# Performance work log

Hardware: AMD Instinct MI355X
Metric: run time of the kernel (lower is better)

Reference implementation:

```python
import jax, jax.numpy as jnp
import numpy as np

E = 8        # n_routed_experts
K = 2        # n_experts_per_token
H = 1024     # d_hidden
D = 512      # d_expert
NSH = 2      # n_shared_experts -> shared expert width = D*NSH


def setup_inputs() -> dict:
    key = jax.random.key(0)
    ks = jax.random.split(key, 8)
    s = 0.02
    x = jax.random.normal(ks[0], (4, 2048, H), jnp.float32)
    W_router = (jax.random.normal(ks[1], (H, E), jnp.float32) * s)
    Wg = (jax.random.normal(ks[2], (E, H, D), jnp.float32) * s)   # per-expert gate proj
    Wu = (jax.random.normal(ks[3], (E, H, D), jnp.float32) * s)   # per-expert up proj
    Wd = (jax.random.normal(ks[4], (E, D, H), jnp.float32) * s)   # per-expert down proj
    Ds = D * NSH
    Wsg = (jax.random.normal(ks[5], (H, Ds), jnp.float32) * s)
    Wsu = (jax.random.normal(ks[6], (H, Ds), jnp.float32) * s)
    Wsd = (jax.random.normal(ks[7], (Ds, H), jnp.float32) * s)
    return {"x": x, "W_router": W_router, "Wg": Wg, "Wu": Wu, "Wd": Wd,
            "Wsg": Wsg, "Wsu": Wsu, "Wsd": Wsd}


def reference(x, W_router, Wg, Wu, Wd, Wsg, Wsu, Wsd):
    B, S, Hd = x.shape
    T = B * S
    xf = x.reshape(T, Hd)

    # shared expert (SwiGLU)
    shared = (jax.nn.silu(xf @ Wsg) * (xf @ Wsu)) @ Wsd          # [T, H]

    # gating: softmax -> top-k -> renormalize
    logits = xf @ W_router                                        # [T, E]
    probs = jax.nn.softmax(logits, axis=-1)
    topk_scores, topk_idx = jax.lax.top_k(probs, K)               # [T, K]
    topk_scores = topk_scores / jnp.sum(topk_scores, axis=-1, keepdims=True)

    # combine weights: zero for unselected experts (topk indices are distinct,
    # so the original's first-match score selection equals a simple scatter)
    combine = jnp.zeros((T, E), x.dtype).at[jnp.arange(T)[:, None], topk_idx].set(topk_scores)

    # per-expert SwiGLU, computed densely and combined with sparse weights
    gate = jax.nn.silu(jnp.einsum('th,ehd->etd', xf, Wg))         # [E, T, D]
    up = jnp.einsum('th,ehd->etd', xf, Wu)                        # [E, T, D]
    expert_out = jnp.einsum('etd,edh->eth', gate * up, Wd)        # [E, T, H]
    routed = jnp.einsum('eth,te->th', expert_out, combine)        # [T, H]

    out = (routed + shared).reshape(B, S, Hd)

    # load-balancing aux loss: E * sum(mean_probs^2)
    probs_mean = jnp.mean(probs.reshape(B, S, E), axis=(0, 1))
    aux_loss = E * jnp.sum(probs_mean * probs_mean)
    return out, aux_loss
```

## Files before the change

kernel.cpp:

```cpp
#include <hip/hip_runtime.h>


typedef unsigned short u16;
typedef unsigned int   u32;
typedef short short8 __attribute__((ext_vector_type(8)));
typedef float f32x4  __attribute__((ext_vector_type(4)));

#define AS1 __attribute__((address_space(1)))
#define AS3 __attribute__((address_space(3)))

constexpr int T  = 8192;
constexpr int H  = 1024;
constexpr int E  = 8;
constexpr int D  = 512;
constexpr int DS = 1024;
constexpr int PAIR_CAP  = 17408;
constexpr int MT_ROUTED = 136;
constexpr int RB = 256;

__device__ __forceinline__ u16 f2bf(float f){
  u32 u = __builtin_bit_cast(u32, f);
  u += 0x7fffu + ((u >> 16) & 1u);
  return (u16)(u >> 16);
}
__device__ __forceinline__ float bf2f(u16 h){
  u32 u = ((u32)h) << 16;
  return __builtin_bit_cast(float, u);
}

__device__ __forceinline__ void gl_lds16(const u16* g, u16* l){
  __builtin_amdgcn_global_load_lds((const AS1 void*)g, (AS3 void*)l, 16, 0, 0);
}

template<int ROWS>
__device__ __forceinline__ void stage_tile(const u16* __restrict__ gbase, int ld, int k0,
                                           int rowbase, const int* __restrict__ gather,
                                           u16* lds, int wave, int lane){
  constexpr int ISS = ROWS / 32;
  int lr = lane >> 3, ch = lane & 7;
  int chs = (ch ^ lr) * 8;
#pragma unroll
  for (int j = 0; j < ISS; ++j){
    int idx = wave * ISS + j;
    int row = idx * 8 + lr;
    int grow = gather ? gather[rowbase + row] : (rowbase + row);
    const u16* g = gbase + (long)grow * ld + k0 + chs;
    gl_lds16(g, lds + idx * 512);
  }
}

__device__ __forceinline__ int swz_off(int c, int lane){
  return ((c ^ (lane & 7)) * 8);
}

__global__ void __launch_bounds__(256) router_kernel(
    const float* __restrict__ x, const float* __restrict__ Wr,
    u16* __restrict__ xb,
    int* __restrict__ topk_idx, float* __restrict__ topk_w,
    int* __restrict__ partial_hist, float* __restrict__ partial_probs)
{
  __shared__ int   hist_s[4][8];
  __shared__ float ps_s[4][8];
  int tid = threadIdx.x, lane = tid & 63, wv = tid >> 6;
  int   histl[8] = {0,0,0,0,0,0,0,0};
  float psl[8]   = {0.f,0.f,0.f,0.f,0.f,0.f,0.f,0.f};

  for (int it = 0; it < 8; ++it){
    int t = blockIdx.x * 32 + wv * 8 + it;
    const float4* xr = (const float4*)(x + (long)t * H);
    uint2* xbr = (uint2*)(xb + (long)t * H);
    float acc[8];
#pragma unroll
    for (int e = 0; e < 8; ++e) acc[e] = 0.f;
#pragma unroll
    for (int i = 0; i < 4; ++i){
      float4 xv = xr[i * 64 + lane];
      u32 lo = (u32)f2bf(xv.x) | ((u32)f2bf(xv.y) << 16);
      u32 hi = (u32)f2bf(xv.z) | ((u32)f2bf(xv.w) << 16);
      xbr[i * 64 + lane] = make_uint2(lo, hi);
      int h0 = i * 256 + lane * 4;
#pragma unroll
      for (int j = 0; j < 4; ++j){
        float xs = (j == 0) ? xv.x : (j == 1) ? xv.y : (j == 2) ? xv.z : xv.w;
        const float4* wr = (const float4*)(Wr + (long)(h0 + j) * E);
        float4 w0 = wr[0], w1 = wr[1];
        acc[0] += xs * w0.x; acc[1] += xs * w0.y; acc[2] += xs * w0.z; acc[3] += xs * w0.w;
        acc[4] += xs * w1.x; acc[5] += xs * w1.y; acc[6] += xs * w1.z; acc[7] += xs * w1.w;
      }
    }
#pragma unroll
    for (int off = 32; off >= 1; off >>= 1){
#pragma unroll
      for (int e = 0; e < 8; ++e) acc[e] += __shfl_xor(acc[e], off, 64);
    }
    if (lane == 0){
      float m = acc[0];
#pragma unroll
      for (int e = 1; e < 8; ++e) m = fmaxf(m, acc[e]);
      float p[8], s = 0.f;
#pragma unroll
      for (int e = 0; e < 8; ++e){ p[e] = __expf(acc[e] - m); s += p[e]; }
      float inv = 1.f / s;
#pragma unroll
      for (int e = 0; e < 8; ++e) psl[e] += p[e] * inv;
      int i1 = 0; float v1 = p[0];
#pragma unroll
      for (int e = 1; e < 8; ++e) if (p[e] > v1){ v1 = p[e]; i1 = e; }
      int i2 = -1; float v2 = -1.f;
#pragma unroll
      for (int e = 0; e < 8; ++e) if (e != i1 && p[e] > v2){ v2 = p[e]; i2 = e; }
      float rs = 1.f / (v1 + v2);
      topk_idx[2 * t] = i1; topk_idx[2 * t + 1] = i2;
      topk_w[2 * t] = v1 * rs; topk_w[2 * t + 1] = v2 * rs;
      histl[i1]++; histl[i2]++;
    }
  }
  if (lane == 0){
#pragma unroll
    for (int e = 0; e < 8; ++e){ hist_s[wv][e] = histl[e]; ps_s[wv][e] = psl[e]; }
  }
  __syncthreads();
  if (tid < 8){
    int hs = 0; float ps = 0.f;
#pragma unroll
    for (int w = 0; w < 4; ++w){ hs += hist_s[w][tid]; ps += ps_s[w][tid]; }
    partial_hist[blockIdx.x * 8 + tid]  = hs;
    partial_probs[blockIdx.x * 8 + tid] = ps;
  }
}

__global__ void __launch_bounds__(64) scan_kernel(
    const int* __restrict__ partial_hist, const float* __restrict__ partial_probs,
    int* __restrict__ block_offset, float* __restrict__ out_aux)
{
  __shared__ int   csum[8][8];
  __shared__ float cps[8][8];
  __shared__ int   cbase[8][8];
  __shared__ int   base_s[8];
  int tid = threadIdx.x, e = tid & 7, c = tid >> 3;
  int s = 0; float f = 0.f;
  for (int b = c * 32; b < c * 32 + 32; ++b){
    s += partial_hist[b * 8 + e]; f += partial_probs[b * 8 + e];
  }
  csum[c][e] = s; cps[c][e] = f;
  __syncthreads();
  if (tid < 8){
    int tot = 0;
    for (int cc = 0; cc < 8; ++cc){ cbase[cc][tid] = tot; tot += csum[cc][tid]; }
    csum[0][tid] = tot;
  }
  __syncthreads();
  if (tid == 0){
    int off = 0;
    for (int ee = 0; ee < 8; ++ee){ base_s[ee] = off; off += (csum[0][ee] + 127) & ~127; }
    float a = 0.f;
    for (int ee = 0; ee < 8; ++ee){
      float ps = 0.f;
      for (int cc = 0; cc < 8; ++cc) ps += cps[cc][ee];
      float m = ps * (1.f / (float)T);
      a += m * m;
    }
    out_aux[0] = (float)E * a;
  }
  __syncthreads();
  int run = base_s[e] + cbase[c][e];
  for (int b = c * 32; b < c * 32 + 32; ++b){
    block_offset[b * 8 + e] = run;
    run += partial_hist[b * 8 + e];
  }
}

__global__ void __launch_bounds__(64) scatter_kernel(
    const int* __restrict__ topk_idx, const float* __restrict__ topk_w,
    const int* __restrict__ block_offset,
    int* __restrict__ pair_token, int* __restrict__ pair_expert,
    float* __restrict__ pair_score, int* __restrict__ token_pos)
{
  int lane = threadIdx.x, b = blockIdx.x;
  int idx = b * 64 + lane;
  int t = idx >> 1;
  int e = topk_idx[idx];
  float w = topk_w[idx];
  unsigned long long below = lane ? ((1ull << lane) - 1ull) : 0ull;
  int rank = 0, basee = 0;
#pragma unroll
  for (int ee = 0; ee < 8; ++ee){
    unsigned long long m = __ballot(e == ee);
    if (e == ee){ rank = __popcll(m & below); basee = block_offset[b * 8 + ee]; }
  }
  int pos = basee + rank;
  pair_token[pos] = t;
  pair_expert[pos] = e;
  pair_score[pos] = w;
  token_pos[idx] = pos;
}

__device__ __forceinline__ void transpose_body(const float* src, u16* dst, int R, int C,
                                               int bz){
  __shared__ float tile[32][33];
  long zoff = (long)bz * R * C;
  int tx = threadIdx.x & 31, ty = threadIdx.x >> 5;
  int c = blockIdx.x * 32 + tx;
  int rb = blockIdx.y * 32;
#pragma unroll
  for (int j = 0; j < 4; ++j)
    tile[ty + j * 8][tx] = src[zoff + (long)(rb + ty + j * 8) * C + c];
  __syncthreads();
#pragma unroll
  for (int j = 0; j < 4; ++j){
    int cc = blockIdx.x * 32 + ty + j * 8;
    dst[zoff + (long)cc * R + rb + tx] = f2bf(tile[tx][ty + j * 8]);
  }
}

__global__ void __launch_bounds__(256) transpose_kernel(const float* __restrict__ src,
                                                        u16* __restrict__ dst, int R, int C){
  transpose_body(src, dst, R, C, blockIdx.z);
}

__global__ void __launch_bounds__(256) transpose2_kernel(
    const float* __restrict__ s0, u16* __restrict__ d0,
    const float* __restrict__ s1, u16* __restrict__ d1, int R, int C, int Z){
  int z = blockIdx.z;
  if (z < Z) transpose_body(s0, d0, R, C, z);
  else       transpose_body(s1, d1, R, C, z - Z);
}

__global__ void __launch_bounds__(256) transpose3_kernel(
    const float* __restrict__ s0, u16* __restrict__ d0,
    const float* __restrict__ s1, u16* __restrict__ d1,
    const float* __restrict__ s2, u16* __restrict__ d2, int R, int C){
  int z = blockIdx.z;
  const float* s = (z == 0) ? s0 : (z == 1) ? s1 : s2;
  u16* d = (z == 0) ? d0 : (z == 1) ? d1 : d2;
  transpose_body(s, d, R, C, 0);
}

__global__ void __launch_bounds__(256) gateup_kernel(
    const u16* __restrict__ A, const u16* __restrict__ Bg, const u16* __restrict__ Bu,
    u16* __restrict__ Hout, int N, int K,
    const int* __restrict__ gather, const int* __restrict__ pexp, long bstride)
{
  __shared__ u16 As[128 * 64];
  __shared__ u16 Bgs[64 * 64];
  __shared__ u16 Bus[64 * 64];
  int tid = threadIdx.x, lane = tid & 63, wave = tid >> 6;
  int wy = wave >> 1, wx = wave & 1;
  int m0 = blockIdx.y * 128, n0 = blockIdx.x * 64;
  int e = pexp ? pexp[m0] : 0;
  const u16* bg = Bg + (long)e * bstride;
  const u16* bu = Bu + (long)e * bstride;
  int rl = lane & 15, q = lane >> 4;

  f32x4 accG[4][2], accU[4][2];
#pragma unroll
  for (int i = 0; i < 4; ++i)
#pragma unroll
    for (int j = 0; j < 2; ++j)
#pragma unroll
      for (int r = 0; r < 4; ++r){ accG[i][j][r] = 0.f; accU[i][j][r] = 0.f; }

  for (int k0 = 0; k0 < K; k0 += 64){
    stage_tile<128>(A, K, k0, m0, gather, As, wave, lane);
    stage_tile<64>(bg, K, k0, n0, nullptr, Bgs, wave, lane);
    stage_tile<64>(bu, K, k0, n0, nullptr, Bus, wave, lane);
    __syncthreads();
#pragma unroll
    for (int ks = 0; ks < 2; ++ks){
      int off = swz_off(ks * 4 + q, lane);
      short8 a[4], g2[2], u2[2];
#pragma unroll
      for (int mt = 0; mt < 4; ++mt)
        a[mt] = *(const short8*)(As + (wy * 64 + mt * 16 + rl) * 64 + off);
#pragma unroll
      for (int nt = 0; nt < 2; ++nt){
        g2[nt] = *(const short8*)(Bgs + (wx * 32 + nt * 16 + rl) * 64 + off);
        u2[nt] = *(const short8*)(Bus + (wx * 32 + nt * 16 + rl) * 64 + off);
      }
#pragma unroll
      for (int mt = 0; mt < 4; ++mt)
#pragma unroll
        for (int nt = 0; nt < 2; ++nt){
          accG[mt][nt] = __builtin_amdgcn_mfma_f32_16x16x32_bf16(a[mt], g2[nt], accG[mt][nt], 0, 0, 0);
          accU[mt][nt] = __builtin_amdgcn_mfma_f32_16x16x32_bf16(a[mt], u2[nt], accU[mt][nt], 0, 0, 0);
        }
    }
    __syncthreads();
  }
  int row0 = m0 + wy * 64, col0 = n0 + wx * 32;
#pragma unroll
  for (int mt = 0; mt < 4; ++mt)
#pragma unroll
    for (int nt = 0; nt < 2; ++nt)
#pragma unroll
      for (int r = 0; r < 4; ++r){
        int row = row0 + mt * 16 + q * 4 + r;
        int col = col0 + nt * 16 + rl;
        float g = accG[mt][nt][r], u = accU[mt][nt][r];
        float h = g / (1.f + __expf(-g)) * u;
        Hout[(long)row * N + col] = f2bf(h);
      }
}

__global__ void __launch_bounds__(256) down_routed_kernel(
    const u16* __restrict__ A, const u16* __restrict__ B, u16* __restrict__ rout,
    const float* __restrict__ pair_score, const int* __restrict__ pexp)
{
  __shared__ u16 As[128 * 64];
  __shared__ u16 Bs[128 * 64];
  int tid = threadIdx.x, lane = tid & 63, wave = tid >> 6;
  int wy = wave >> 1, wx = wave & 1;
  int m0 = blockIdx.y * 128, n0 = blockIdx.x * 128;
  int e = pexp[m0];
  const u16* b = B + (long)e * (H * D);
  int rl = lane & 15, q = lane >> 4;

  f32x4 acc[4][4];
#pragma unroll
  for (int i = 0; i < 4; ++i)
#pragma unroll
    for (int j = 0; j < 4; ++j)
#pragma unroll
      for (int r = 0; r < 4; ++r) acc[i][j][r] = 0.f;

  for (int k0 = 0; k0 < D; k0 += 64){
    stage_tile<128>(A, D, k0, m0, nullptr, As, wave, lane);
    stage_tile<128>(b, D, k0, n0, nullptr, Bs, wave, lane);
    __syncthreads();
#pragma unroll
    for (int ks = 0; ks < 2; ++ks){
      int off = swz_off(ks * 4 + q, lane);
      short8 a[4], bv[4];
#pragma unroll
      for (int mt = 0; mt < 4; ++mt)
        a[mt] = *(const short8*)(As + (wy * 64 + mt * 16 + rl) * 64 + off);
#pragma unroll
      for (int nt = 0; nt < 4; ++nt)
        bv[nt] = *(const short8*)(Bs + (wx * 64 + nt * 16 + rl) * 64 + off);
#pragma unroll
      for (int mt = 0; mt < 4; ++mt)
#pragma unroll
        for (int nt = 0; nt < 4; ++nt)
          acc[mt][nt] = __builtin_amdgcn_mfma_f32_16x16x32_bf16(a[mt], bv[nt], acc[mt][nt], 0, 0, 0);
    }
    __syncthreads();
  }
#pragma unroll
  for (int mt = 0; mt < 4; ++mt)
#pragma unroll
    for (int r = 0; r < 4; ++r){
      int row = m0 + wy * 64 + mt * 16 + q * 4 + r;
      float s = pair_score[row];
      long rbase = (long)row * H;
#pragma unroll
      for (int nt = 0; nt < 4; ++nt){
        int col = n0 + wx * 64 + nt * 16 + rl;
        rout[rbase + col] = f2bf(s * acc[mt][nt][r]);
      }
    }
}

__global__ void __launch_bounds__(256) down_shared_kernel(
    const u16* __restrict__ A, const u16* __restrict__ B,
    const u16* __restrict__ rout, const int* __restrict__ token_pos,
    float* __restrict__ out)
{
  __shared__ u16 As[128 * 64];
  __shared__ u16 Bs[128 * 64];
  int tid = threadIdx.x, lane = tid & 63, wave = tid >> 6;
  int wy = wave >> 1, wx = wave & 1;
  int m0 = blockIdx.y * 128, n0 = blockIdx.x * 128;
  int rl = lane & 15, q = lane >> 4;

  f32x4 acc[4][4];
#pragma unroll
  for (int i = 0; i < 4; ++i)
#pragma unroll
    for (int j = 0; j < 4; ++j)
#pragma unroll
      for (int r = 0; r < 4; ++r) acc[i][j][r] = 0.f;

  for (int k0 = 0; k0 < DS; k0 += 64){
    stage_tile<128>(A, DS, k0, m0, nullptr, As, wave, lane);
    stage_tile<128>(B, DS, k0, n0, nullptr, Bs, wave, lane);
    __syncthreads();
#pragma unroll
    for (int ks = 0; ks < 2; ++ks){
      int off = swz_off(ks * 4 + q, lane);
      short8 a[4], bv[4];
#pragma unroll
      for (int mt = 0; mt < 4; ++mt)
        a[mt] = *(const short8*)(As + (wy * 64 + mt * 16 + rl) * 64 + off);
#pragma unroll
      for (int nt = 0; nt < 4; ++nt)
        bv[nt] = *(const short8*)(Bs + (wx * 64 + nt * 16 + rl) * 64 + off);
#pragma unroll
      for (int mt = 0; mt < 4; ++mt)
#pragma unroll
        for (int nt = 0; nt < 4; ++nt)
          acc[mt][nt] = __builtin_amdgcn_mfma_f32_16x16x32_bf16(a[mt], bv[nt], acc[mt][nt], 0, 0, 0);
    }
    __syncthreads();
  }
#pragma unroll
  for (int mt = 0; mt < 4; ++mt)
#pragma unroll
    for (int r = 0; r < 4; ++r){
      int row = m0 + wy * 64 + mt * 16 + q * 4 + r;
      int p0 = token_pos[2 * row], p1 = token_pos[2 * row + 1];
      long o = (long)row * H;
#pragma unroll
      for (int nt = 0; nt < 4; ++nt){
        int col = n0 + wx * 64 + nt * 16 + rl;
        out[o + col] = acc[mt][nt][r]
                     + bf2f(rout[(long)p0 * H + col])
                     + bf2f(rout[(long)p1 * H + col]);
      }
    }
}

extern "C" void kernel_launch(void* const* d_in, const int* in_sizes, int n_in,
                              void* d_out, int out_size, void* d_ws, size_t ws_size,
                              hipStream_t stream)
{
  (void)in_sizes; (void)n_in; (void)out_size; (void)ws_size;
  const float* x   = (const float*)d_in[0];
  const float* Wr  = (const float*)d_in[1];
  const float* Wg  = (const float*)d_in[2];
  const float* Wu  = (const float*)d_in[3];
  const float* Wd  = (const float*)d_in[4];
  const float* Wsg = (const float*)d_in[5];
  const float* Wsu = (const float*)d_in[6];
  const float* Wsd = (const float*)d_in[7];
  float* out = (float*)d_out;

  char* ws = (char*)d_ws;
  size_t off = 0;
  auto alloc = [&](size_t bytes) -> void* {
    void* p = ws + off; off += (bytes + 255) & ~(size_t)255; return p;
  };
  u16* xb   = (u16*)alloc((size_t)T * H * 2);
  u16* WsgT = (u16*)alloc((size_t)DS * H * 2);
  u16* WsuT = (u16*)alloc((size_t)DS * H * 2);
  u16* WsdT = (u16*)alloc((size_t)H * DS * 2);
  u16* WgT  = (u16*)alloc((size_t)E * D * H * 2);
  u16* WuT  = (u16*)alloc((size_t)E * D * H * 2);
  u16* WdT  = (u16*)alloc((size_t)E * H * D * 2);
  u16* hs   = (u16*)alloc((size_t)T * DS * 2);
  u16* hr   = (u16*)alloc((size_t)PAIR_CAP * D * 2);
  u16* rout = (u16*)alloc((size_t)PAIR_CAP * H * 2);
  int*   topk_idx  = (int*)alloc((size_t)T * 2 * 4);
  float* topk_w    = (float*)alloc((size_t)T * 2 * 4);
  int*   token_pos = (int*)alloc((size_t)T * 2 * 4);
  int*   partial_hist  = (int*)alloc((size_t)RB * 8 * 4);
  float* partial_probs = (float*)alloc((size_t)RB * 8 * 4);
  int*   block_offset  = (int*)alloc((size_t)RB * 8 * 4);
  char* zbase = ws + off;
  int*   pair_token  = (int*)alloc((size_t)PAIR_CAP * 4);
  int*   pair_expert = (int*)alloc((size_t)PAIR_CAP * 4);
  float* pair_score  = (float*)alloc((size_t)PAIR_CAP * 4);
  size_t zbytes = (size_t)((ws + off) - zbase);

  hipMemsetAsync(zbase, 0, zbytes, stream);

  transpose3_kernel<<<dim3(32, 32, 3), 256, 0, stream>>>(
      Wsg, WsgT, Wsu, WsuT, Wsd, WsdT, 1024, 1024);
  transpose2_kernel<<<dim3(D / 32, H / 32, 2 * E), 256, 0, stream>>>(
      Wg, WgT, Wu, WuT, H, D, E);
  transpose_kernel<<<dim3(H / 32, D / 32, E), 256, 0, stream>>>(Wd, WdT, D, H);

  router_kernel<<<RB, 256, 0, stream>>>(x, Wr, xb, topk_idx, topk_w,
                                        partial_hist, partial_probs);
  scan_kernel<<<1, 64, 0, stream>>>(partial_hist, partial_probs, block_offset,
                                    out + (size_t)T * H);
  scatter_kernel<<<RB, 64, 0, stream>>>(topk_idx, topk_w, block_offset,
                                        pair_token, pair_expert, pair_score, token_pos);

  gateup_kernel<<<dim3(DS / 64, T / 128), 256, 0, stream>>>(
      xb, WsgT, WsuT, hs, DS, H, nullptr, nullptr, 0);
  gateup_kernel<<<dim3(D / 64, MT_ROUTED), 256, 0, stream>>>(
      xb, WgT, WuT, hr, D, H, pair_token, pair_expert, (long)D * H);
  down_routed_kernel<<<dim3(H / 128, MT_ROUTED), 256, 0, stream>>>(
      hr, WdT, rout, pair_score, pair_expert);
  down_shared_kernel<<<dim3(H / 128, T / 128), 256, 0, stream>>>(
      hs, WsdT, rout, token_pos, out);
}
```

Measured before the change: 352.5 us.

## Double-buffer LDS tiles with async prefetch and XCD-aware block remap

The GEMM kernels (gate/up, routed down, shared down) now keep two LDS buffers. The next K-tile's global-to-LDS loads are issued before the current tile is computed, using explicit vmcnt waits and lighter barriers in place of full syncthreads. Block indices are remapped so consecutive blocks on the same XCD share M-tiles, which should improve L2 reuse. Row pointers are precomputed once per block. Doubling LDS use may reduce occupancy, and the remap assumes the M-tile count is a multiple of 8.

```diff
diff --git a/kernel.cpp b/kernel.cpp
--- a/kernel.cpp
+++ b/kernel.cpp
@@ -32,10 +32,30 @@
   __builtin_amdgcn_global_load_lds((const AS1 void*)g, (AS3 void*)l, 16, 0, 0);
 }
 
+__device__ __forceinline__ void wait_vmcnt8(){ __builtin_amdgcn_s_waitcnt(0x0f78); }
+__device__ __forceinline__ void wait_vmcnt0(){ __builtin_amdgcn_s_waitcnt(0x0f70); }
+
+__device__ __forceinline__ void bar_sync(){
+  __builtin_amdgcn_fence(__ATOMIC_RELEASE, "workgroup", "local");
+  __builtin_amdgcn_s_barrier();
+  __builtin_amdgcn_fence(__ATOMIC_ACQUIRE, "workgroup", "local");
+}
+
+__device__ __forceinline__ void xcd_remap(int& mtile, int& ntile){
+  int NT = gridDim.x;
+  int lid = blockIdx.y * NT + blockIdx.x;
+  int x8 = lid & 7, s = lid >> 3;
+  mtile = x8 + 8 * (s / NT);
+  ntile = s % NT;
+}
+
+template<int ISS>
+struct StagePtr { const u16* p[ISS]; };
+
 template<int ROWS>
-__device__ __forceinline__ void stage_tile(const u16* __restrict__ gbase, int ld, int k0,
-                                           int rowbase, const int* __restrict__ gather,
-                                           u16* lds, int wave, int lane){
+__device__ __forceinline__ void stage_init(StagePtr<ROWS/32>& sp,
+    const u16* __restrict__ gbase, int ld, int rowbase,
+    const int* __restrict__ gather, int wave, int lane){
   constexpr int ISS = ROWS / 32;
   int lr = lane >> 3, ch = lane & 7;
   int chs = (ch ^ lr) * 8;
@@ -44,9 +64,17 @@
     int idx = wave * ISS + j;
     int row = idx * 8 + lr;
     int grow = gather ? gather[rowbase + row] : (rowbase + row);
-    const u16* g = gbase + (long)grow * ld + k0 + chs;
-    gl_lds16(g, lds + idx * 512);
-  }
+    sp.p[j] = gbase + (long)grow * ld + chs;
+  }
+}
+
+template<int ROWS>
+__device__ __forceinline__ void stage_issue(const StagePtr<ROWS/32>& sp, int k0,
+                                            u16* lds, int wave, int lane){
+  constexpr int ISS = ROWS / 32;
+#pragma unroll
+  for (int j = 0; j < ISS; ++j)
+    gl_lds16(sp.p[j] + k0, lds + (wave * ISS + j) * 512);
 }
 
 __device__ __forceinline__ int swz_off(int c, int lane){
@@ -241,17 +269,23 @@
     u16* __restrict__ Hout, int N, int K,
     const int* __restrict__ gather, const int* __restrict__ pexp, long bstride)
 {
-  __shared__ u16 As[128 * 64];
-  __shared__ u16 Bgs[64 * 64];
-  __shared__ u16 Bus[64 * 64];
+  __shared__ u16 As[2][128 * 64];
+  __shared__ u16 Bgs[2][64 * 64];
+  __shared__ u16 Bus[2][64 * 64];
   int tid = threadIdx.x, lane = tid & 63, wave = tid >> 6;
   int wy = wave >> 1, wx = wave & 1;
-  int m0 = blockIdx.y * 128, n0 = blockIdx.x * 64;
+  int mtile, ntile; xcd_remap(mtile, ntile);
+  int m0 = mtile * 128, n0 = ntile * 64;
   int e = pexp ? pexp[m0] : 0;
   const u16* bg = Bg + (long)e * bstride;
   const u16* bu = Bu + (long)e * bstride;
   int rl = lane & 15, q = lane >> 4;
 
+  StagePtr<4> spA; StagePtr<2> spG; StagePtr<2> spU;
+  stage_init<128>(spA, A, K, m0, gather, wave, lane);
+  stage_init<64>(spG, bg, K, n0, nullptr, wave, lane);
+  stage_init<64>(spU, bu, K, n0, nullptr, wave, lane);
+
   f32x4 accG[4][2], accU[4][2];
 #pragma unroll
   for (int i = 0; i < 4; ++i)
@@ -260,22 +294,34 @@
 #pragma unroll
       for (int r = 0; r < 4; ++r){ accG[i][j][r] = 0.f; accU[i][j][r] = 0.f; }
 
-  for (int k0 = 0; k0 < K; k0 += 64){
-    stage_tile<128>(A, K, k0, m0, gather, As, wave, lane);
-    stage_tile<64>(bg, K, k0, n0, nullptr, Bgs, wave, lane);
-    stage_tile<64>(bu, K, k0, n0, nullptr, Bus, wave, lane);
-    __syncthreads();
+  stage_issue<128>(spA, 0, As[0], wave, lane);
+  stage_issue<64>(spG, 0, Bgs[0], wave, lane);
+  stage_issue<64>(spU, 0, Bus[0], wave, lane);
+
+  int NI = K / 64;
+  for (int i = 0; i < NI; ++i){
+    int cur = i & 1, nxt = cur ^ 1;
+    if (i + 1 < NI){
+      int kn = (i + 1) * 64;
+      stage_issue<128>(spA, kn, As[nxt], wave, lane);
+      stage_issue<64>(spG, kn, Bgs[nxt], wave, lane);
+      stage_issue<64>(spU, kn, Bus[nxt], wave, lane);
+      wait_vmcnt8();
+    } else {
+      wait_vmcnt0();
+    }
+    bar_sync();
 #pragma unroll
     for (int ks = 0; ks < 2; ++ks){
       int off = swz_off(ks * 4 + q, lane);
       short8 a[4], g2[2], u2[2];
 #pragma unroll
       for (int mt = 0; mt < 4; ++mt)
-        a[mt] = *(const short8*)(As + (wy * 64 + mt * 16 + rl) * 64 + off);
+        a[mt] = *(const short8*)(As[cur] + (wy * 64 + mt * 16 + rl) * 64 + off);
 #pragma unroll
       for (int nt = 0; nt < 2; ++nt){
-        g2[nt] = *(const short8*)(Bgs + (wx * 32 + nt * 16 + rl) * 64 + off);
-        u2[nt] = *(const short8*)(Bus + (wx * 32 + nt * 16 + rl) * 64 + off);
+        g2[nt] = *(const short8*)(Bgs[cur] + (wx * 32 + nt * 16 + rl) * 64 + off);
+        u2[nt] = *(const short8*)(Bus[cur] + (wx * 32 + nt * 16 + rl) * 64 + off);
       }
 #pragma unroll
       for (int mt = 0; mt < 4; ++mt)
@@ -285,7 +331,7 @@
           accU[mt][nt] = __builtin_amdgcn_mfma_f32_16x16x32_bf16(a[mt], u2[nt], accU[mt][nt], 0, 0, 0);
         }
     }
-    __syncthreads();
+    if (i + 1 < NI) bar_sync();
   }
   int row0 = m0 + wy * 64, col0 = n0 + wx * 32;
 #pragma unroll
@@ -302,62 +348,102 @@
       }
 }
 
+template<bool ROUTED>
+__device__ __forceinline__ void down_body(
+    const u16* __restrict__ A, const u16* __restrict__ Bbase, int K,
+    u16* __restrict__ rout, const float* __restrict__ pair_score,
+    const int* __restrict__ token_pos, float* __restrict__ out)
+{
+  __shared__ u16 As[2][128 * 64];
+  __shared__ u16 Bs[2][128 * 64];
+  int tid = threadIdx.x, lane = tid & 63, wave = tid >> 6;
+  int wy = wave >> 1, wx = wave & 1;
+  int mtile, ntile; xcd_remap(mtile, ntile);
+  int m0 = mtile * 128, n0 = ntile * 128;
+  int rl = lane & 15, q = lane >> 4;
+
+  StagePtr<4> spA, spB;
+  stage_init<128>(spA, A, K, m0, nullptr, wave, lane);
+  stage_init<128>(spB, Bbase, K, n0, nullptr, wave, lane);
+
+  f32x4 acc[4][4];
+#pragma unroll
+  for (int i = 0; i < 4; ++i)
+#pragma unroll
+    for (int j = 0; j < 4; ++j)
+#pragma unroll
+      for (int r = 0; r < 4; ++r) acc[i][j][r] = 0.f;
+
+  stage_issue<128>(spA, 0, As[0], wave, lane);
+  stage_issue<128>(spB, 0, Bs[0], wave, lane);
+
+  int NI = K / 64;
+  for (int i = 0; i < NI; ++i){
+    int cur = i & 1, nxt = cur ^ 1;
+    if (i + 1 < NI){
+      int kn = (i + 1) * 64;
+      stage_issue<128>(spA, kn, As[nxt], wave, lane);
+      stage_issue<128>(spB, kn, Bs[nxt], wave, lane);
+      wait_vmcnt8();
+    } else {
+      wait_vmcnt0();
+    }
+    bar_sync();
+#pragma unroll
+    for (int ks = 0; ks < 2; ++ks){
+      int off = swz_off(ks * 4 + q, lane);
+      short8 a[4], bv[4];
+#pragma unroll
+      for (int mt = 0; mt < 4; ++mt)
+        a[mt] = *(const short8*)(As[cur] + (wy * 64 + mt * 16 + rl) * 64 + off);
+#pragma unroll
+      for (int nt = 0; nt < 4; ++nt)
+        bv[nt] = *(const short8*)(Bs[cur] + (wx * 64 + nt * 16 + rl) * 64 + off);
+#pragma unroll
+      for (int mt = 0; mt < 4; ++mt)
+#pragma unroll
+        for (int nt = 0; nt < 4; ++nt)
+          acc[mt][nt] = __builtin_amdgcn_mfma_f32_16x16x32_bf16(a[mt], bv[nt], acc[mt][nt], 0, 0, 0);
+    }
+    if (i + 1 < NI) bar_sync();
+  }
+#pragma unroll
+  for (int mt = 0; mt < 4; ++mt)
+#pragma unroll
+    for (int r = 0; r < 4; ++r){
+      int row = m0 + wy * 64 + mt * 16 + q * 4 + r;
+      if (ROUTED){
+        float s = pair_score[row];
+        long rbase = (long)row * H;
+#pragma unroll
+        for (int nt = 0; nt < 4; ++nt){
+          int col = n0 + wx * 64 + nt * 16 + rl;
+          rout[rbase + col] = f2bf(s * acc[mt][nt][r]);
+        }
+      } else {
+        int p0 = token_pos[2 * row], p1 = token_pos[2 * row + 1];
+        long o = (long)row * H;
+#pragma unroll
+        for (int nt = 0; nt < 4; ++nt){
+          int col = n0 + wx * 64 + nt * 16 + rl;
+          out[o + col] = acc[mt][nt][r]
+                       + bf2f(rout[(long)p0 * H + col])
+                       + bf2f(rout[(long)p1 * H + col]);
+        }
+      }
+    }
+}
+
 __global__ void __launch_bounds__(256) down_routed_kernel(
     const u16* __restrict__ A, const u16* __restrict__ B, u16* __restrict__ rout,
     const float* __restrict__ pair_score, const int* __restrict__ pexp)
 {
-  __shared__ u16 As[128 * 64];
-  __shared__ u16 Bs[128 * 64];
-  int tid = threadIdx.x, lane = tid & 63, wave = tid >> 6;
-  int wy = wave >> 1, wx = wave & 1;
-  int m0 = blockIdx.y * 128, n0 = blockIdx.x * 128;
-  int e = pexp[m0];
-  const u16* b = B + (long)e * (H * D);
-  int rl = lane & 15, q = lane >> 4;
-
-  f32x4 acc[4][4];
-#pragma unroll
-  for (int i = 0; i < 4; ++i)
-#pragma unroll
-    for (int j = 0; j < 4; ++j)
-#pragma unroll
-      for (int r = 0; r < 4; ++r) acc[i][j][r] = 0.f;
-
-  for (int k0 = 0; k0 < D; k0 += 64){
-    stage_tile<128>(A, D, k0, m0, nullptr, As, wave, lane);
-    stage_tile<128>(b, D, k0, n0, nullptr, Bs, wave, lane);
-    __syncthreads();
-#pragma unroll
-    for (int ks = 0; ks < 2; ++ks){
-      int off = swz_off(ks * 4 + q, lane);
-      short8 a[4], bv[4];
-#pragma unroll
-      for (int mt = 0; mt < 4; ++mt)
-        a[mt] = *(const short8*)(As + (wy * 64 + mt * 16 + rl) * 64 + off);
-#pragma unroll
-      for (int nt = 0; nt < 4; ++nt)
-        bv[nt] = *(const short8*)(Bs + (wx * 64 + nt * 16 + rl) * 64 + off);
-#pragma unroll
-      for (int mt = 0; mt < 4; ++mt)
-#pragma unroll
-        for (int nt = 0; nt < 4; ++nt)
-          acc[mt][nt] = __builtin_amdgcn_mfma_f32_16x16x32_bf16(a[mt], bv[nt], acc[mt][nt], 0, 0, 0);
-    }
-    __syncthreads();
-  }
-#pragma unroll
-  for (int mt = 0; mt < 4; ++mt)
-#pragma unroll
-    for (int r = 0; r < 4; ++r){
-      int row = m0 + wy * 64 + mt * 16 + q * 4 + r;
-      float s = pair_score[row];
-      long rbase = (long)row * H;
-#pragma unroll
-      for (int nt = 0; nt < 4; ++nt){
-        int col = n0 + wx * 64 + nt * 16 + rl;
-        rout[rbase + col] = f2bf(s * acc[mt][nt][r]);
-      }
-    }
+  int NT = gridDim.x;
+  int lid = blockIdx.y * NT + blockIdx.x;
+  int x8 = lid & 7, s = lid >> 3;
+  int mtile = x8 + 8 * (s / NT);
+  int e = pexp[mtile * 128];
+  down_body<true>(A, B + (long)e * (H * D), D, rout, pair_score, nullptr, nullptr);
 }
 
 __global__ void __launch_bounds__(256) down_shared_kernel(
@@ -365,58 +451,7 @@
     const u16* __restrict__ rout, const int* __restrict__ token_pos,
     float* __restrict__ out)
 {
-  __shared__ u16 As[128 * 64];
-  __shared__ u16 Bs[128 * 64];
-  int tid = threadIdx.x, lane = tid & 63, wave = tid >> 6;
-  int wy = wave >> 1, wx = wave & 1;
-  int m0 = blockIdx.y * 128, n0 = blockIdx.x * 128;
-  int rl = lane & 15, q = lane >> 4;
-
-  f32x4 acc[4][4];
-#pragma unroll
-  for (int i = 0; i < 4; ++i)
-#pragma unroll
-    for (int j = 0; j < 4; ++j)
-#pragma unroll
-      for (int r = 0; r < 4; ++r) acc[i][j][r] = 0.f;
-
-  for (int k0 = 0; k0 < DS; k0 += 64){
-    stage_tile<128>(A, DS, k0, m0, nullptr, As, wave, lane);
-    stage_tile<128>(B, DS, k0, n0, nullptr, Bs, wave, lane);
-    __syncthreads();
-#pragma unroll
-    for (int ks = 0; ks < 2; ++ks){
-      int off = swz_off(ks * 4 + q, lane);
-      short8 a[4], bv[4];
-#pragma unroll
-      for (int mt = 0; mt < 4; ++mt)
-        a[mt] = *(const short8*)(As + (wy * 64 + mt * 16 + rl) * 64 + off);
-#pragma unroll
-      for (int nt = 0; nt < 4; ++nt)
-        bv[nt] = *(const short8*)(Bs + (wx * 64 + nt * 16 + rl) * 64 + off);
-#pragma unroll
-      for (int mt = 0; mt < 4; ++mt)
-#pragma unroll
-        for (int nt = 0; nt < 4; ++nt)
-          acc[mt][nt] = __builtin_amdgcn_mfma_f32_16x16x32_bf16(a[mt], bv[nt], acc[mt][nt], 0, 0, 0);
-    }
-    __syncthreads();
-  }
-#pragma unroll
-  for (int mt = 0; mt < 4; ++mt)
-#pragma unroll
-    for (int r = 0; r < 4; ++r){
-      int row = m0 + wy * 64 + mt * 16 + q * 4 + r;
-      int p0 = token_pos[2 * row], p1 = token_pos[2 * row + 1];
-      long o = (long)row * H;
-#pragma unroll
-      for (int nt = 0; nt < 4; ++nt){
-        int col = n0 + wx * 64 + nt * 16 + rl;
-        out[o + col] = acc[mt][nt][r]
-                     + bf2f(rout[(long)p0 * H + col])
-                     + bf2f(rout[(long)p1 * H + col]);
-      }
-    }
+  down_body<false>(A, B, DS, const_cast<u16*>(rout), nullptr, token_pos, out);
 }
 
 extern "C" void kernel_launch(void* const* d_in, const int* in_sizes, int n_in,
```

Result: faster. 329.9 us (-6.4%).
